# Kernel optimization log

Measured on AMD Instinct MI355X. Metric: run time of the kernel, lower is better.

The kernel has to match this reference:

```python
import jax, jax.numpy as jnp
import numpy as np

N = 100000  # nodes
E = 1600000  # edges
D_IN, D_HID, D_OUT = 128, 128, 64
NEG_SLOPE = 0.2


def gat_conv(x, src, dst, W_src, W_dst, att_src, att_dst, bias, num_nodes):
    # PyG GATConv, heads=1, add_self_loops=False.
    h_src = x @ W_src          # [N, C]
    h_dst = x @ W_dst          # [N, C]
    a_src = (h_src * att_src).sum(-1)   # [N]
    a_dst = (h_dst * att_dst).sum(-1)   # [N]
    logits = jax.nn.leaky_relu(a_src[src] + a_dst[dst], NEG_SLOPE)  # [E]
    # segment softmax over destination neighborhoods
    seg_max = jax.ops.segment_max(logits, dst, num_segments=num_nodes)  # [N]
    e = jnp.exp(logits - seg_max[dst])
    denom = jax.ops.segment_sum(e, dst, num_segments=num_nodes)         # [N]
    alpha = e / (denom[dst] + 1e-16)                                    # [E]
    out = jax.ops.segment_sum(alpha[:, None] * h_src[src], dst, num_segments=num_nodes)  # [N, C]
    return out + bias


def setup_inputs() -> dict:
    key = jax.random.key(0)
    ks = jax.random.split(key, 12)
    x = jax.random.normal(ks[0], (N, D_IN), dtype=jnp.float32)
    edge_index = jax.random.randint(ks[1], (2, E), 0, N, dtype=jnp.int64)
    s1 = 1.0 / np.sqrt(D_IN)
    s2 = 1.0 / np.sqrt(D_HID)
    return {
        "x": x,
        "edge_index": edge_index,
        "W1_src": jax.random.uniform(ks[2], (D_IN, D_HID), jnp.float32, -s1, s1),
        "W1_dst": jax.random.uniform(ks[3], (D_IN, D_HID), jnp.float32, -s1, s1),
        "att1_src": jax.random.uniform(ks[4], (D_HID,), jnp.float32, -s2, s2),
        "att1_dst": jax.random.uniform(ks[5], (D_HID,), jnp.float32, -s2, s2),
        "b1": jnp.zeros((D_HID,), jnp.float32),
        "W2_src": jax.random.uniform(ks[6], (D_HID, D_OUT), jnp.float32, -s2, s2),
        "W2_dst": jax.random.uniform(ks[7], (D_HID, D_OUT), jnp.float32, -s2, s2),
        "att2_src": jax.random.uniform(ks[8], (D_OUT,), jnp.float32, -1.0 / np.sqrt(D_OUT), 1.0 / np.sqrt(D_OUT)),
        "att2_dst": jax.random.uniform(ks[9], (D_OUT,), jnp.float32, -1.0 / np.sqrt(D_OUT), 1.0 / np.sqrt(D_OUT)),
        "b2": jnp.zeros((D_OUT,), jnp.float32),
    }


def reference(x, edge_index, W1_src, W1_dst, att1_src, att1_dst, b1,
              W2_src, W2_dst, att2_src, att2_dst, b2):
    src, dst = edge_index[0], edge_index[1]
    h = gat_conv(x, src, dst, W1_src, W1_dst, att1_src, att1_dst, b1, N)
    h = jax.nn.relu(h)
    out = gat_conv(h, src, dst, W2_src, W2_dst, att2_src, att2_dst, b2, N)
    return out
```

## Files before the change

### kernel.cpp

```cpp
#include <hip/hip_runtime.h>


typedef unsigned long long u64;
typedef float v4f __attribute__((ext_vector_type(4)));
typedef _Float16 v2h __attribute__((ext_vector_type(2)));
typedef __fp16 h8 __attribute__((ext_vector_type(8)));

#define SEL_LO 0x01000504u
#define SEL_HI 0x03020706u

__device__ __forceinline__ void ntstore4(float* p, v4f v) {
    __builtin_nontemporal_store(v, (v4f*)p);
}
__device__ __forceinline__ unsigned h2pack(float a, float b) {
    v2h h;
    h.x = (_Float16)a;
    h.y = (_Float16)b;
    return __builtin_bit_cast(unsigned, h);
}
__device__ __forceinline__ float fdot2u(unsigned u, v2h w, float acc) {
    return __builtin_amdgcn_fdot2(__builtin_bit_cast(v2h, u), w, acc, false);
}
__device__ __forceinline__ v2h pkrtz(float a, float b) {
    return __builtin_bit_cast(v2h, __builtin_amdgcn_cvt_pkrtz(a, b));
}

__global__ __launch_bounds__(64) void matvec_kernel(const float* __restrict__ W,
                                                    const float* __restrict__ a,
                                                    float* __restrict__ out, int cols) {
    int row = blockIdx.x;
    int lane = threadIdx.x;
    float s = 0.f;
    for (int j = lane; j < cols; j += 64) s += W[row * cols + j] * a[j];
#pragma unroll
    for (int o = 32; o; o >>= 1) s += __shfl_xor(s, o, 64);
    if (lane == 0) out[row] = s;
}

template <int C>
__global__ __launch_bounds__(256) void packw_kernel(const float* __restrict__ W,
                                                    uint4* __restrict__ Wp) {
    constexpr int NT = C / 16;
    const int total = 4 * NT * 64;
    for (int e = threadIdx.x; e < total; e += 256) {
        int lane = e & 63;
        int ti = (e >> 6) % NT;
        int t = (e >> 6) / NT;
        int k0 = 32 * t + (lane >> 4) * 8;
        int n = ti * 16 + (lane & 15);
        unsigned u[4];
#pragma unroll
        for (int p = 0; p < 4; ++p)
            u[p] = h2pack(W[(size_t)(k0 + 2 * p) * C + n], W[(size_t)(k0 + 2 * p + 1) * C + n]);
        Wp[e] = make_uint4(u[0], u[1], u[2], u[3]);
    }
}

__global__ __launch_bounds__(256) void bhist_kernel(const int* __restrict__ dst,
                                                    int* __restrict__ gh, int E) {
    __shared__ int h[256];
    h[threadIdx.x] = 0;
    __syncthreads();
    int base = blockIdx.x * 4096;
    int lim = min(base + 4096, E);
    for (int i = base + threadIdx.x; i < lim; i += 256)
        atomicAdd(&h[__builtin_nontemporal_load(dst + i) >> 9], 1);
    __syncthreads();
    int v = h[threadIdx.x];
    if (v) atomicAdd(&gh[threadIdx.x], v);
}

__global__ __launch_bounds__(256) void bscan_kernel(const int* __restrict__ gh,
                                                    int* __restrict__ bbase,
                                                    int* __restrict__ gcur,
                                                    int* __restrict__ offs, int N, int E) {
    __shared__ int s[256];
    int t = threadIdx.x;
    int v = gh[t];
    s[t] = v;
    __syncthreads();
    for (int o = 1; o < 256; o <<= 1) {
        int u = (t >= o) ? s[t - o] : 0;
        __syncthreads();
        s[t] += u;
        __syncthreads();
    }
    int excl = s[t] - v;
    bbase[t] = excl;
    gcur[t] = excl;
    if (t == 255) { bbase[256] = E; offs[N] = E; }
}

__global__ __launch_bounds__(256) void bscatter_kernel(const int* __restrict__ src,
                                                       const int* __restrict__ dst,
                                                       int* __restrict__ gcur,
                                                       u64* __restrict__ pairs, int E) {
    __shared__ int h[256];
    __shared__ int rbase[256];
    const int tid = threadIdx.x;
    h[tid] = 0;
    __syncthreads();
    const int base = blockIdx.x * 4096;
    u64 pv[16];
    int rk[16];
    int bk[16];
#pragma unroll 16
    for (int k = 0; k < 16; ++k) {
        int i = base + k * 256 + tid;
        if (i < E) {
            int d = __builtin_nontemporal_load(dst + i);
            int b = d >> 9;
            bk[k] = b;
            pv[k] = ((u64)(unsigned)d << 32) | (unsigned)__builtin_nontemporal_load(src + i);
            rk[k] = atomicAdd(&h[b], 1);
        } else {
            bk[k] = -1;
        }
    }
    __syncthreads();
    int c = h[tid];
    rbase[tid] = c ? atomicAdd(&gcur[tid], c) : 0;
    __syncthreads();
#pragma unroll 16
    for (int k = 0; k < 16; ++k)
        if (bk[k] >= 0)
            __builtin_nontemporal_store(pv[k], pairs + (size_t)rbase[bk[k]] + rk[k]);
}

__global__ __launch_bounds__(512) void bsort_kernel(const u64* __restrict__ pairs,
                                                    const int* __restrict__ bbase,
                                                    int* __restrict__ offs,
                                                    int* __restrict__ srcs, int N) {
    __shared__ int h[512];
    __shared__ int cur[512];
    const int t = threadIdx.x;
    const int b = blockIdx.x;
    const int beg = bbase[b], end = bbase[b + 1];
    h[t] = 0;
    __syncthreads();
    for (int i = beg + t; i < end; i += 512)
        atomicAdd(&h[(int)(__builtin_nontemporal_load(pairs + i) >> 32) & 511], 1);
    __syncthreads();
    int v = h[t];
    cur[t] = v;
    __syncthreads();
    for (int o = 1; o < 512; o <<= 1) {
        int u = (t >= o) ? cur[t - o] : 0;
        __syncthreads();
        cur[t] += u;
        __syncthreads();
    }
    int pos0 = beg + cur[t] - v;
    __syncthreads();
    cur[t] = pos0;
    int g = (b << 9) + t;
    if (g < N) offs[g] = pos0;
    __syncthreads();
    for (int i = beg + t; i < end; i += 512) {
        u64 p = __builtin_nontemporal_load(pairs + i);
        int local = (int)(p >> 32) & 511;
        int pp = atomicAdd(&cur[local], 1);
        srcs[pp] = (int)(p & 0xffffffffu);
    }
}

template <int C, bool XF16>
__global__ __launch_bounds__(256) void gemm_att_kernel(
    const void* __restrict__ Xv, const uint4* __restrict__ Wp,
    const float* __restrict__ attS, const float* __restrict__ wda,
    unsigned* __restrict__ H, float* __restrict__ aS, float* __restrict__ aD, int M) {
    constexpr int NT = C / 16;
    __shared__ _Float16 hs[4][16 * 136];

    const int tid = threadIdx.x;
    const int w = tid >> 6;
    const int lane = tid & 63;
    const int l15 = lane & 15;
    const int q = lane >> 4;
    const int mb = blockIdx.x * 64 + w * 16;
    const int m = mb + l15;
    const bool mv = m < M;

    v4f acc[NT];
#pragma unroll
    for (int n = 0; n < NT; ++n) acc[n] = (v4f)(0.f);
    float pd = 0.f;
    uint4 afu[4];

    if constexpr (XF16) {
        const uint4* Xp = (const uint4*)Xv + (size_t)m * 16;
#pragma unroll
        for (int t = 0; t < 4; ++t) {
            uint4 u = make_uint4(0u, 0u, 0u, 0u);
            if (mv) u = Xp[4 * t + q];
            afu[t] = u;
            const float* wdp = wda + 32 * t + 8 * q;
            pd = fdot2u(u.x, pkrtz(wdp[0], wdp[1]), pd);
            pd = fdot2u(u.y, pkrtz(wdp[2], wdp[3]), pd);
            pd = fdot2u(u.z, pkrtz(wdp[4], wdp[5]), pd);
            pd = fdot2u(u.w, pkrtz(wdp[6], wdp[7]), pd);
        }
    } else {
        const float* Xp = (const float*)Xv + (size_t)m * 128;
#pragma unroll
        for (int t = 0; t < 4; ++t) {
            float4 x0 = make_float4(0.f, 0.f, 0.f, 0.f);
            float4 x1 = x0;
            if (mv) {
                x0 = *(const float4*)(Xp + 32 * t + 8 * q);
                x1 = *(const float4*)(Xp + 32 * t + 8 * q + 4);
            }
            const float* wdp = wda + 32 * t + 8 * q;
            pd += x0.x * wdp[0] + x0.y * wdp[1] + x0.z * wdp[2] + x0.w * wdp[3] +
                  x1.x * wdp[4] + x1.y * wdp[5] + x1.z * wdp[6] + x1.w * wdp[7];
            afu[t] = make_uint4(h2pack(x0.x, x0.y), h2pack(x0.z, x0.w),
                                h2pack(x1.x, x1.y), h2pack(x1.z, x1.w));
        }
    }

#pragma unroll
    for (int t = 0; t < 4; ++t) {
        h8 a = __builtin_bit_cast(h8, afu[t]);
        const uint4* wp = Wp + (size_t)t * NT * 64 + lane;
#pragma unroll
        for (int n = 0; n < NT; ++n) {
            h8 b = __builtin_bit_cast(h8, wp[n * 64]);
            acc[n] = __builtin_amdgcn_mfma_f32_16x16x32_f16(a, b, acc[n], 0, 0, 0);
        }
    }

    pd += __shfl_xor(pd, 16, 64);
    pd += __shfl_xor(pd, 32, 64);
    if (q == 0 && mv) aD[m] = pd;

    float as4[4] = {0.f, 0.f, 0.f, 0.f};
#pragma unroll
    for (int n = 0; n < NT; ++n) {
        float av = attS[n * 16 + l15];
#pragma unroll
        for (int r = 0; r < 4; ++r) as4[r] += acc[n][r] * av;
    }
#pragma unroll
    for (int r = 0; r < 4; ++r) {
#pragma unroll
        for (int o = 1; o < 16; o <<= 1) as4[r] += __shfl_xor(as4[r], o, 64);
    }
    if (l15 == 0) {
#pragma unroll
        for (int r = 0; r < 4; ++r) {
            int row = mb + q * 4 + r;
            if (row < M) aS[row] = as4[r];
        }
    }

    _Float16* hp = hs[w];
#pragma unroll
    for (int n = 0; n < NT; ++n)
#pragma unroll
        for (int r = 0; r < 4; ++r)
            hp[(q * 4 + r) * 136 + n * 16 + l15] = (_Float16)acc[n][r];

    constexpr int CH = C / 32;
    if (lane < 16 * CH) {
        int row = lane / CH;
        int ch = lane % CH;
        const uint4* rp = (const uint4*)(hp + row * 136 + ch * 32);
        uint4 v0 = rp[0], v1 = rp[1], v2 = rp[2], v3 = rp[3];
        int gr = mb + row;
        if (gr < M) {
            uint4* op = (uint4*)(H + (size_t)gr * (C / 2)) + ch * 4;
            op[0] = v0; op[1] = v1; op[2] = v2; op[3] = v3;
        }
    }
}

template <int C, bool RELU, bool F16OUT, bool NTOUT>
__global__ __launch_bounds__(256) void aggregate_kernel(
    const int* __restrict__ offs, const int* __restrict__ srcs,
    const unsigned* __restrict__ hsrc, const float* __restrict__ aS,
    const float* __restrict__ aD, const float* __restrict__ bias,
    void* __restrict__ outv, int n) {
    const int lane = threadIdx.x & 63;
    const int sl = lane & 31;
    const int hb = lane & 32;
    const int g = (lane >> 4) & 1;
    const int l = lane & 15;
    int node = (int)((blockIdx.x * blockDim.x + threadIdx.x) >> 5);
    if (node >= n) return;

    const int beg = offs[node], end = offs[node + 1];
    const int deg = end - beg;
    const float ad = aD[node];

    constexpr int LW = C / 32;
    constexpr int NA = C / 16;
    float acc[NA];
#pragma unroll
    for (int i = 0; i < NA; ++i) acc[i] = 0.f;

    int sj = 0;
    float u = 0.f;

    auto ldrow = [&](int s, unsigned* r) {
        if constexpr (C == 128) {
            uint4 v = ((const uint4*)(hsrc + ((size_t)s << 6)))[l];
            r[0] = v.x; r[1] = v.y; r[2] = v.z; r[3] = v.w;
        } else {
            uint2 v = ((const uint2*)(hsrc + ((size_t)s << 5)))[l];
            r[0] = v.x; r[1] = v.y;
        }
    };
    auto issue = [&](int j, unsigned (*buf)[LW]) {
        int e0 = hb + j * 8 + g;
        int s0 = __shfl(sj, e0, 64);
        int s1 = __shfl(sj, e0 + 2, 64);
        int s2 = __shfl(sj, e0 + 4, 64);
        int s3 = __shfl(sj, e0 + 6, 64);
        ldrow(s0, buf[0]);
        ldrow(s1, buf[1]);
        ldrow(s2, buf[2]);
        ldrow(s3, buf[3]);
    };
    auto compute = [&](int j, unsigned (*buf)[LW], float inv) {
        int e0 = hb + j * 8 + g;
        float w0 = __shfl(u, e0, 64) * inv, w1 = __shfl(u, e0 + 2, 64) * inv;
        float w2 = __shfl(u, e0 + 4, 64) * inv, w3 = __shfl(u, e0 + 6, 64) * inv;
        v2h w01 = pkrtz(w0, w1);
        v2h w23 = pkrtz(w2, w3);
#pragma unroll
        for (int ii = 0; ii < LW; ++ii) {
            acc[2 * ii] = fdot2u(__builtin_amdgcn_perm(buf[0][ii], buf[1][ii], SEL_LO), w01,
                          fdot2u(__builtin_amdgcn_perm(buf[2][ii], buf[3][ii], SEL_LO), w23, acc[2 * ii]));
            acc[2 * ii + 1] = fdot2u(__builtin_amdgcn_perm(buf[0][ii], buf[1][ii], SEL_HI), w01,
                              fdot2u(__builtin_amdgcn_perm(buf[2][ii], buf[3][ii], SEL_HI), w23, acc[2 * ii + 1]));
        }
    };

    unsigned A0[4][LW], A1[4][LW];

    if (deg <= 32) {
        int i = beg + sl;
        if (i < end) {
            sj = __builtin_nontemporal_load(srcs + i);
            float lg = aS[sj] + ad;
            lg = (lg > 0.f) ? lg : 0.2f * lg;
            u = __expf(lg);
        }
        int jm = (deg + 7) >> 3;
        if (jm > 0) issue(0, A0);
        if (jm > 1) issue(1, A1);
        float s = u;
#pragma unroll
        for (int o = 16; o; o >>= 1) s += __shfl_xor(s, o, 64);
        float inv = 1.f / (s + 1e-16f);
        if (jm > 0) { compute(0, A0, inv); if (jm > 2) issue(2, A0); }
        if (jm > 1) { compute(1, A1, inv); if (jm > 3) issue(3, A1); }
        if (jm > 2) compute(2, A0, inv);
        if (jm > 3) compute(3, A1, inv);
    } else {
        float m = -INFINITY;
        for (int i = beg + sl; i < end; i += 32) {
            float lg = aS[srcs[i]] + ad;
            lg = (lg > 0.f) ? lg : 0.2f * lg;
            m = fmaxf(m, lg);
        }
#pragma unroll
        for (int o = 16; o; o >>= 1) m = fmaxf(m, __shfl_xor(m, o, 64));
        float ssum = 0.f;
        for (int i = beg + sl; i < end; i += 32) {
            float lg = aS[srcs[i]] + ad;
            lg = (lg > 0.f) ? lg : 0.2f * lg;
            ssum += __expf(lg - m);
        }
#pragma unroll
        for (int o = 16; o; o >>= 1) ssum += __shfl_xor(ssum, o, 64);
        float inv = 1.f / (ssum + 1e-16f);
        for (int base = beg; base < end; base += 32) {
            int i = base + sl;
            sj = 0;
            u = 0.f;
            if (i < end) {
                sj = srcs[i];
                float lg = aS[sj] + ad;
                lg = (lg > 0.f) ? lg : 0.2f * lg;
                u = __expf(lg - m);
            }
            int cnt = min(32, end - base);
            int cj = (cnt + 7) >> 3;
            if (cj > 0) issue(0, A0);
            if (cj > 1) issue(1, A1);
            if (cj > 0) { compute(0, A0, inv); if (cj > 2) issue(2, A0); }
            if (cj > 1) { compute(1, A1, inv); if (cj > 3) issue(3, A1); }
            if (cj > 2) compute(2, A0, inv);
            if (cj > 3) compute(3, A1, inv);
        }
    }

#pragma unroll
    for (int i = 0; i < NA; ++i) acc[i] += __shfl_xor(acc[i], 16, 64);

    if (sl < 16) {
        float o[NA];
        const float* bp = bias + l * NA;
#pragma unroll
        for (int i = 0; i < NA; ++i) {
            o[i] = acc[i] + bp[i];
            if (RELU) o[i] = fmaxf(o[i], 0.f);
        }
        if constexpr (F16OUT) {
            unsigned uo[NA / 2];
#pragma unroll
            for (int k = 0; k < NA / 2; ++k) uo[k] = h2pack(o[2 * k], o[2 * k + 1]);
            unsigned* op = (unsigned*)outv + (size_t)node * (C / 2) + l * (NA / 2);
            if constexpr (NA == 8) *(uint4*)op = make_uint4(uo[0], uo[1], uo[2], uo[3]);
            else *(uint2*)op = make_uint2(uo[0], uo[1]);
        } else {
            float* op = (float*)outv + (size_t)node * C + l * NA;
#pragma unroll
            for (int q = 0; q < NA / 4; ++q) {
                v4f ov;
                ov.x = o[q * 4 + 0]; ov.y = o[q * 4 + 1];
                ov.z = o[q * 4 + 2]; ov.w = o[q * 4 + 3];
                if (NTOUT) ntstore4(op + q * 4, ov);
                else *(v4f*)(op + q * 4) = ov;
            }
        }
    }
}

extern "C" void kernel_launch(void* const* d_in, const int* in_sizes, int n_in,
                              void* d_out, int out_size, void* d_ws, size_t ws_size,
                              hipStream_t stream) {
    const float* x     = (const float*)d_in[0];
    const int*   edge  = (const int*)d_in[1];
    const float* W1s   = (const float*)d_in[2];
    const float* W1d   = (const float*)d_in[3];
    const float* att1s = (const float*)d_in[4];
    const float* att1d = (const float*)d_in[5];
    const float* b1    = (const float*)d_in[6];
    const float* W2s   = (const float*)d_in[7];
    const float* W2d   = (const float*)d_in[8];
    const float* att2s = (const float*)d_in[9];
    const float* att2d = (const float*)d_in[10];
    const float* b2    = (const float*)d_in[11];

    const int N = in_sizes[0] / 128;
    const int E = in_sizes[1] / 2;
    const int* srcI = edge;
    const int* dstI = edge + E;

    size_t off = 0;
    auto alloc = [&](size_t bytes) {
        void* p = (char*)d_ws + off;
        off += (bytes + 255) & ~(size_t)255;
        return p;
    };
    int*      offs  = (int*)alloc((size_t)(N + 1) * 4);
    int*      srcs  = (int*)alloc((size_t)E * 4);
    int*      gh    = (int*)alloc(256 * 4);
    int*      bbase = (int*)alloc(257 * 4);
    int*      gcur  = (int*)alloc(256 * 4);
    float*    watt1 = (float*)alloc(128 * 4);
    float*    watt2 = (float*)alloc(128 * 4);
    uint4*    wp1   = (uint4*)alloc(4 * 8 * 64 * 16);
    uint4*    wp2   = (uint4*)alloc(4 * 4 * 64 * 16);
    float*    a_s   = (float*)alloc((size_t)N * 4);
    float*    a_d   = (float*)alloc((size_t)N * 4);
    unsigned* g1h   = (unsigned*)alloc((size_t)N * 128 * 2);
    unsigned* h1h   = (unsigned*)alloc((size_t)N * 128 * 2);
    unsigned* g2h   = (unsigned*)alloc((size_t)N * 64 * 2);
    u64*      pairs = (u64*)h1h;

    hipMemsetAsync(gh, 0, 256 * 4, stream);
    matvec_kernel<<<128, 64, 0, stream>>>(W1d, att1d, watt1, 128);
    matvec_kernel<<<128, 64, 0, stream>>>(W2d, att2d, watt2, 64);
    packw_kernel<128><<<1, 256, 0, stream>>>(W1s, wp1);
    packw_kernel<64><<<1, 256, 0, stream>>>(W2s, wp2);

    const int nbE = (E + 4095) / 4096;
    const int nbuckets = (N + 511) >> 9;
    bhist_kernel<<<nbE, 256, 0, stream>>>(dstI, gh, E);
    bscan_kernel<<<1, 256, 0, stream>>>(gh, bbase, gcur, offs, N, E);
    bscatter_kernel<<<nbE, 256, 0, stream>>>(srcI, dstI, gcur, pairs, E);
    bsort_kernel<<<nbuckets, 512, 0, stream>>>(pairs, bbase, offs, srcs, N);

    int gblk = (N + 63) / 64;
    gemm_att_kernel<128, false><<<gblk, 256, 0, stream>>>(x, wp1, att1s, watt1, g1h, a_s, a_d, N);
    aggregate_kernel<128, true, true, false><<<(N + 7) / 8, 256, 0, stream>>>(
        offs, srcs, g1h, a_s, a_d, b1, h1h, N);
    gemm_att_kernel<64, true><<<gblk, 256, 0, stream>>>(h1h, wp2, att2s, watt2, g2h, a_s, a_d, N);
    aggregate_kernel<64, false, false, true><<<(N + 7) / 8, 256, 0, stream>>>(
        offs, srcs, g2h, a_s, a_d, b2, d_out, N);
}
```

Before: 327.4 us.

## Stage bucket scatter in LDS and issue all gather loads upfront

The bucket scatter kernel now prefix-sums its per-block bucket counts, stages the pairs sorted by bucket in a 32KB shared buffer, and writes them out in order so global stores are contiguous per bucket instead of scattered. The aggregation kernel uses four register buffers instead of two, issuing all neighbor row gathers before computing the softmax weights, and moves the attention-score load earlier so its latency overlaps with the gathers. This raises LDS use (which may lower occupancy of the scatter kernel) and register pressure in the aggregation kernel, which could reduce occupancy.

```diff
diff --git a/kernel.cpp b/kernel.cpp
--- a/kernel.cpp
+++ b/kernel.cpp
@@ -96,11 +96,14 @@
                                                        int* __restrict__ gcur,
                                                        u64* __restrict__ pairs, int E) {
     __shared__ int h[256];
+    __shared__ int sbase[256];
     __shared__ int rbase[256];
+    __shared__ u64 buf[4096];
     const int tid = threadIdx.x;
     h[tid] = 0;
     __syncthreads();
     const int base = blockIdx.x * 4096;
+    const int lim = min(4096, E - base);
     u64 pv[16];
     int rk[16];
     int bk[16];
@@ -118,13 +121,29 @@
         }
     }
     __syncthreads();
-    int c = h[tid];
-    rbase[tid] = c ? atomicAdd(&gcur[tid], c) : 0;
+    const int v = h[tid];
+    sbase[tid] = v;
+    __syncthreads();
+    for (int o = 1; o < 256; o <<= 1) {
+        int uu = (tid >= o) ? sbase[tid - o] : 0;
+        __syncthreads();
+        sbase[tid] += uu;
+        __syncthreads();
+    }
+    const int excl = sbase[tid] - v;
+    rbase[tid] = v ? atomicAdd(&gcur[tid], v) : 0;
+    __syncthreads();
+    sbase[tid] = excl;
     __syncthreads();
 #pragma unroll 16
     for (int k = 0; k < 16; ++k)
-        if (bk[k] >= 0)
-            __builtin_nontemporal_store(pv[k], pairs + (size_t)rbase[bk[k]] + rk[k]);
+        if (bk[k] >= 0) buf[sbase[bk[k]] + rk[k]] = pv[k];
+    __syncthreads();
+    for (int i = tid; i < lim; i += 256) {
+        u64 p = buf[i];
+        int b = (int)(p >> 41);
+        __builtin_nontemporal_store(p, pairs + (size_t)rbase[b] + (i - sbase[b]));
+    }
 }
 
 __global__ __launch_bounds__(512) void bsort_kernel(const u64* __restrict__ pairs,
@@ -336,27 +355,30 @@
         }
     };
 
-    unsigned A0[4][LW], A1[4][LW];
+    unsigned A0[4][LW], A1[4][LW], A2[4][LW], A3[4][LW];
 
     if (deg <= 32) {
         int i = beg + sl;
-        if (i < end) {
-            sj = __builtin_nontemporal_load(srcs + i);
-            float lg = aS[sj] + ad;
-            lg = (lg > 0.f) ? lg : 0.2f * lg;
-            u = __expf(lg);
-        }
+        if (i < end) sj = __builtin_nontemporal_load(srcs + i);
+        float asv = (i < end) ? aS[sj] : 0.f;
         int jm = (deg + 7) >> 3;
         if (jm > 0) issue(0, A0);
         if (jm > 1) issue(1, A1);
+        if (jm > 2) issue(2, A2);
+        if (jm > 3) issue(3, A3);
+        if (i < end) {
+            float lg = asv + ad;
+            lg = (lg > 0.f) ? lg : 0.2f * lg;
+            u = __expf(lg);
+        }
         float s = u;
 #pragma unroll
         for (int o = 16; o; o >>= 1) s += __shfl_xor(s, o, 64);
         float inv = 1.f / (s + 1e-16f);
-        if (jm > 0) { compute(0, A0, inv); if (jm > 2) issue(2, A0); }
-        if (jm > 1) { compute(1, A1, inv); if (jm > 3) issue(3, A1); }
-        if (jm > 2) compute(2, A0, inv);
-        if (jm > 3) compute(3, A1, inv);
+        if (jm > 0) compute(0, A0, inv);
+        if (jm > 1) compute(1, A1, inv);
+        if (jm > 2) compute(2, A2, inv);
+        if (jm > 3) compute(3, A3, inv);
     } else {
         float m = -INFINITY;
         for (int i = beg + sl; i < end; i += 32) {
@@ -389,10 +411,12 @@
             int cj = (cnt + 7) >> 3;
             if (cj > 0) issue(0, A0);
             if (cj > 1) issue(1, A1);
-            if (cj > 0) { compute(0, A0, inv); if (cj > 2) issue(2, A0); }
-            if (cj > 1) { compute(1, A1, inv); if (cj > 3) issue(3, A1); }
-            if (cj > 2) compute(2, A0, inv);
-            if (cj > 3) compute(3, A1, inv);
+            if (cj > 2) issue(2, A2);
+            if (cj > 3) issue(3, A3);
+            if (cj > 0) compute(0, A0, inv);
+            if (cj > 1) compute(1, A1, inv);
+            if (cj > 2) compute(2, A2, inv);
+            if (cj > 3) compute(3, A3, inv);
         }
     }
 
```

New measurement: 312.0 us. 4.7% less time.
